# Optimization experiments

Measured on AMD Instinct MI355X. Metric: run time of the kernel, lower is better.

## Reference

```python
import jax, jax.numpy as jnp
import numpy as np

N = 100000   # nodes
D = 128      # embedding dim
E = 1600000  # edges (avg in-degree 16)
EPS = 1e-15
MAX_TANH_ARG = 1.0 - 1e-7  # keep arctanh finite


def _logmap0(x):
    # Poincare-ball logmap at the origin: artanh(||x||) * x / ||x||
    norm = jnp.linalg.norm(x, axis=-1, keepdims=True)
    safe = jnp.maximum(norm, EPS)
    return jnp.arctanh(jnp.clip(norm, 0.0, MAX_TANH_ARG)) * x / safe


def _expmap0(v):
    # Poincare-ball expmap at the origin: tanh(||v||) * v / ||v||
    norm = jnp.linalg.norm(v, axis=-1, keepdims=True)
    safe = jnp.maximum(norm, EPS)
    return jnp.tanh(norm) * v / safe


def setup_inputs() -> dict:
    key = jax.random.key(0)
    k1, k2, k3, k4, k5 = jax.random.split(key, 5)
    # small norms keep points strictly inside the unit ball
    x = jax.random.normal(k1, (N, D), dtype=jnp.float32) * 0.01
    src = jax.random.randint(k2, (E,), 0, N)
    dst = jax.random.randint(k3, (E,), 0, N)
    W = jax.random.normal(k4, (D, D), dtype=jnp.float32) * (1.0 / np.sqrt(D))
    b = jax.random.normal(k5, (D,), dtype=jnp.float32) * 0.01
    return {"x": x, "W": W, "b": b, "src": src, "dst": dst}


def reference(x, W, b, src, dst):
    # logmap to tangent space at origin
    tangent_x = _logmap0(x)
    # linear layer (nn.Linear: x @ W^T + b)
    h = tangent_x @ W.T + b  # [N, D]
    # copy_u + mean aggregation over in-neighbors (DGL update_all)
    msg_sum = jax.ops.segment_sum(h[src], dst, num_segments=N)      # [N, D]
    deg = jax.ops.segment_sum(jnp.ones((E,), h.dtype), dst, num_segments=N)
    neigh = msg_sum / jnp.maximum(deg, 1.0)[:, None]  # zero-degree nodes -> 0 (DGL mean)
    # expmap back onto the Poincare ball
    return _expmap0(neigh)
```

## Files before the change

### kernel.cpp

```cpp
#include <hip/hip_runtime.h>
#include <hip/hip_fp16.h>
#include <math.h>

constexpr int D = 128;
constexpr int BSH = 9;
constexpr int BNODES = 1 << BSH;
constexpr int NBLK = 256;

typedef __attribute__((ext_vector_type(8))) short bf16x8;
typedef __attribute__((ext_vector_type(4))) float f32x4;

__device__ inline short f2bf(float f) {
    unsigned u = __builtin_bit_cast(unsigned, f);
    u = (u + 0x7FFFu + ((u >> 16) & 1u)) >> 16;
    return (short)u;
}

__global__ __launch_bounds__(256) void hist_tangent_kernel(
    const int* __restrict__ dst, int* __restrict__ blkhist,
    int nEdges, int NB,
    const float* __restrict__ x, __half* __restrict__ th, int nNodes)
{
    __shared__ int hist[256];
    int t = threadIdx.x;

    if (blockIdx.x < NBLK) {
        hist[t] = 0;
        __syncthreads();
        int per = (nEdges + NBLK - 1) / NBLK;
        int i0 = blockIdx.x * per;
        int i1 = min(nEdges, i0 + per);
        for (int i = i0 + t; i < i1; i += 256)
            atomicAdd(&hist[dst[i] >> BSH], 1);
        __syncthreads();
        if (t < NB) blkhist[t * NBLK + blockIdx.x] = hist[t];
        return;
    }

    int nb = blockIdx.x - NBLK;
    int n    = (nb * 256 + t) >> 6;
    int lane = t & 63;
    if (n >= nNodes) return;
    float2 xv = *reinterpret_cast<const float2*>(x + (size_t)n * D + lane * 2);
    float ss = xv.x * xv.x + xv.y * xv.y;
    ss += __shfl_xor(ss, 1);
    ss += __shfl_xor(ss, 2);
    ss += __shfl_xor(ss, 4);
    ss += __shfl_xor(ss, 8);
    ss += __shfl_xor(ss, 16);
    ss += __shfl_xor(ss, 32);
    float norm = sqrtf(ss);
    float ncl  = fminf(norm, 1.0f - 1e-7f);
    float at   = 0.5f * logf((1.0f + ncl) / (1.0f - ncl));
    float sc   = at / fmaxf(norm, 1e-15f);
    __half2 h = __float22half2_rn(make_float2(xv.x * sc, xv.y * sc));
    *(reinterpret_cast<__half2*>(th + (size_t)n * D) + lane) = h;
}

__global__ __launch_bounds__(256) void part_scan1_kernel(
    int* __restrict__ blkhist, int* __restrict__ btot)
{
    __shared__ int s[256];
    int b = blockIdx.x;
    int t = threadIdx.x;
    int v = blkhist[b * NBLK + t];
    s[t] = v;
    __syncthreads();
    for (int off = 1; off < 256; off <<= 1) {
        int xv = (t >= off) ? s[t - off] : 0;
        __syncthreads();
        if (t >= off) s[t] += xv;
        __syncthreads();
    }
    blkhist[b * NBLK + t] = s[t] - v;
    if (t == 255) btot[b] = s[255];
}

__global__ __launch_bounds__(256) void part_scatter_kernel(
    const int* __restrict__ src, const int* __restrict__ dst,
    const int* __restrict__ blkhist, const int* __restrict__ btot,
    unsigned* __restrict__ part, int nEdges, int NB)
{
    __shared__ int sb[256];
    __shared__ int cur[256];
    int t = threadIdx.x;
    int v = (t < NB) ? btot[t] : 0;
    sb[t] = v;
    __syncthreads();
    for (int off = 1; off < 256; off <<= 1) {
        int xv = (t >= off) ? sb[t - off] : 0;
        __syncthreads();
        if (t >= off) sb[t] += xv;
        __syncthreads();
    }
    int bbase_t = sb[t] - v;
    cur[t] = (t < NB) ? (blkhist[t * NBLK + blockIdx.x] + bbase_t) : 0;
    __syncthreads();

    int per = (nEdges + gridDim.x - 1) / gridDim.x;
    int i0 = blockIdx.x * per;
    int i1 = min(nEdges, i0 + per);
    for (int i = i0 + t; i < i1; i += 256) {
        int d = dst[i];
        int b = d >> BSH;
        int p = atomicAdd(&cur[b], 1);
        part[p] = (unsigned)src[i] | ((unsigned)(d & (BNODES - 1)) << 17);
    }
}

__global__ __launch_bounds__(256) void bucket_csr_kernel(
    const unsigned* __restrict__ part, const int* __restrict__ btot,
    int* __restrict__ rowptr, float* __restrict__ degf,
    int* __restrict__ csr_src, int nNodes, int NB, int nEdges)
{
    __shared__ int cnt[BNODES];
    __shared__ int excl[BNODES];
    __shared__ int cur[BNODES];
    __shared__ int s[256];
    __shared__ int sBB[2];

    int b = blockIdx.x;
    int t = threadIdx.x;

    int v = (t < NB) ? btot[t] : 0;
    s[t] = v;
    __syncthreads();
    for (int off = 1; off < 256; off <<= 1) {
        int xv = (t >= off) ? s[t - off] : 0;
        __syncthreads();
        if (t >= off) s[t] += xv;
        __syncthreads();
    }
    if (t == b) { sBB[0] = s[t] - v; sBB[1] = s[t]; }
    __syncthreads();
    int bb = sBB[0], be = sBB[1];

    cnt[t] = 0; cnt[t + 256] = 0;
    cur[t] = 0; cur[t + 256] = 0;
    __syncthreads();

    for (int i = bb + t; i < be; i += 256)
        atomicAdd(&cnt[part[i] >> 17], 1);
    __syncthreads();

    int a0 = cnt[2 * t], a1 = cnt[2 * t + 1];
    s[t] = a0 + a1;
    __syncthreads();
    for (int off = 1; off < 256; off <<= 1) {
        int xv = (t >= off) ? s[t - off] : 0;
        __syncthreads();
        if (t >= off) s[t] += xv;
        __syncthreads();
    }
    int pbase = (t > 0) ? s[t - 1] : 0;
    excl[2 * t]     = pbase;
    excl[2 * t + 1] = pbase + a0;
    __syncthreads();

    int node0 = b << BSH;
#pragma unroll
    for (int q = 0; q < 2; ++q) {
        int j = t + q * 256;
        int d = node0 + j;
        if (d < nNodes) {
            rowptr[d] = bb + excl[j];
            degf[d]   = (float)cnt[j];
        }
    }
    if (b == NB - 1 && t == 0) rowptr[nNodes] = nEdges;

    for (int i = bb + t; i < be; i += 256) {
        unsigned vv = part[i];
        int dloc = vv >> 17;
        int p = bb + excl[dloc] + atomicAdd(&cur[dloc], 1);
        csr_src[p] = (int)(vv & 0x1FFFFu);
    }
}

__global__ __launch_bounds__(256) void hist_win_kernel(
    const int* __restrict__ dst, int* __restrict__ count,
    int nEdges, int winSize)
{
    int pass    = blockIdx.x & 7;
    int slice   = blockIdx.x >> 3;
    int nSlices = gridDim.x >> 3;
    int lo = pass * winSize;
    int hi = lo + winSize;

    int stride = nSlices * blockDim.x;
    for (int i = slice * blockDim.x + threadIdx.x; i < nEdges; i += stride) {
        int d = dst[i];
        if (d >= lo && d < hi) atomicAdd(&count[d], 1);
    }
}

__global__ __launch_bounds__(256) void scan_block_kernel(
    const int* __restrict__ count, int* __restrict__ rowptr,
    int* __restrict__ blksums, int n)
{
    __shared__ int sums[256];
    int t = threadIdx.x;
    int base = blockIdx.x * 1024 + t * 4;
    int v[4];
    int s = 0;
#pragma unroll
    for (int j = 0; j < 4; ++j) { v[j] = (base + j < n) ? count[base + j] : 0; s += v[j]; }
    sums[t] = s;
    __syncthreads();
    for (int off = 1; off < 256; off <<= 1) {
        int xv = (t >= off) ? sums[t - off] : 0;
        __syncthreads();
        if (t >= off) sums[t] += xv;
        __syncthreads();
    }
    int run = (t > 0) ? sums[t - 1] : 0;
#pragma unroll
    for (int j = 0; j < 4; ++j) { if (base + j < n) rowptr[base + j] = run; run += v[j]; }
    if (t == 255) blksums[blockIdx.x] = sums[255];
}

__global__ __launch_bounds__(256) void scan_totals_kernel(
    int* __restrict__ blksums, int* __restrict__ rowptr,
    int numBlocks, int n, int E)
{
    __shared__ int s[256];
    int t = threadIdx.x;
    s[t] = (t < numBlocks) ? blksums[t] : 0;
    __syncthreads();
    for (int off = 1; off < 256; off <<= 1) {
        int xv = (t >= off) ? s[t - off] : 0;
        __syncthreads();
        if (t >= off) s[t] += xv;
        __syncthreads();
    }
    if (t < numBlocks) blksums[t] = (t > 0) ? s[t - 1] : 0;
    if (t == 0) rowptr[n] = E;
}

__global__ __launch_bounds__(256) void add_offsets_kernel(
    int* __restrict__ rowptr, const int* __restrict__ blksums, int n)
{
    int i = blockIdx.x * 256 + threadIdx.x;
    if (i < n) rowptr[i] += blksums[i >> 10];
}

__global__ __launch_bounds__(256) void fill_win_kernel(
    const int* __restrict__ src, const int* __restrict__ dst,
    const int* __restrict__ rowptr, int* __restrict__ count,
    int* __restrict__ csr_src, int nEdges, int winSize)
{
    int pass    = blockIdx.x & 7;
    int slice   = blockIdx.x >> 3;
    int nSlices = gridDim.x >> 3;
    int lo = pass * winSize;
    int hi = lo + winSize;

    int stride = nSlices * blockDim.x;
    for (int i = slice * blockDim.x + threadIdx.x; i < nEdges; i += stride) {
        int d = dst[i];
        if (d >= lo && d < hi) {
            int pos = rowptr[d] + atomicSub(&count[d], 1) - 1;
            csr_src[pos] = src[i];
        }
    }
}

__global__ __launch_bounds__(256) void deg_from_rowptr_kernel(
    const int* __restrict__ rowptr, float* __restrict__ degf, int n)
{
    int i = blockIdx.x * 256 + threadIdx.x;
    if (i < n) degf[i] = (float)(rowptr[i + 1] - rowptr[i]);
}

__global__ __launch_bounds__(256) void scale_kernel(
    const float* __restrict__ x, float* __restrict__ scale, int nNodes)
{
    int node = (blockIdx.x * 256 + threadIdx.x) >> 6;
    int lane = threadIdx.x & 63;
    if (node >= nNodes) return;
    float2 xv = *reinterpret_cast<const float2*>(x + (size_t)node * D + lane * 2);
    float ss = xv.x * xv.x + xv.y * xv.y;
    ss += __shfl_xor(ss, 1);
    ss += __shfl_xor(ss, 2);
    ss += __shfl_xor(ss, 4);
    ss += __shfl_xor(ss, 8);
    ss += __shfl_xor(ss, 16);
    ss += __shfl_xor(ss, 32);
    if (lane == 0) {
        float norm = sqrtf(ss);
        float ncl  = fminf(norm, 1.0f - 1e-7f);
        float at   = 0.5f * logf((1.0f + ncl) / (1.0f - ncl));
        scale[node] = at / fmaxf(norm, 1e-15f);
    }
}

__global__ __launch_bounds__(256) void gather2_h16b_kernel(
    const __half* __restrict__ th,
    const int* __restrict__ csr_src, const int* __restrict__ rowptr,
    short* __restrict__ msgb, int nNodes)
{
    int t    = threadIdx.x;
    int lane = t & 63;
    int wave = t >> 6;
    int grp  = lane >> 4;
    int np   = grp >> 1;
    int g2   = grp & 1;
    int sl   = lane & 15;

    int n  = blockIdx.x * 8 + wave * 2 + np;
    int nn = n < nNodes ? n : nNodes - 1;
    int beg = rowptr[nn];
    int cnt = rowptr[nn + 1] - beg;

    __half2 z = __float2half2_rn(0.0f);
    __half2 acc0[4] = {z, z, z, z};
    __half2 acc1[4] = {z, z, z, z};

    int k = g2;
    for (; k + 6 < cnt; k += 8) {
        int s0 = csr_src[beg + k];
        int s1 = csr_src[beg + k + 2];
        int s2 = csr_src[beg + k + 4];
        int s3 = csr_src[beg + k + 6];
        float4 r0 = *reinterpret_cast<const float4*>(th + (size_t)s0 * D + sl * 8);
        float4 r1 = *reinterpret_cast<const float4*>(th + (size_t)s1 * D + sl * 8);
        float4 r2 = *reinterpret_cast<const float4*>(th + (size_t)s2 * D + sl * 8);
        float4 r3 = *reinterpret_cast<const float4*>(th + (size_t)s3 * D + sl * 8);
        const __half2* h0 = reinterpret_cast<const __half2*>(&r0);
        const __half2* h1 = reinterpret_cast<const __half2*>(&r1);
        const __half2* h2 = reinterpret_cast<const __half2*>(&r2);
        const __half2* h3 = reinterpret_cast<const __half2*>(&r3);
#pragma unroll
        for (int j = 0; j < 4; ++j) {
            acc0[j] = __hadd2(acc0[j], h0[j]);
            acc1[j] = __hadd2(acc1[j], h1[j]);
            acc0[j] = __hadd2(acc0[j], h2[j]);
            acc1[j] = __hadd2(acc1[j], h3[j]);
        }
    }
    for (; k < cnt; k += 2) {
        int s0 = csr_src[beg + k];
        float4 r0 = *reinterpret_cast<const float4*>(th + (size_t)s0 * D + sl * 8);
        const __half2* h0 = reinterpret_cast<const __half2*>(&r0);
#pragma unroll
        for (int j = 0; j < 4; ++j) acc0[j] = __hadd2(acc0[j], h0[j]);
    }
#pragma unroll
    for (int j = 0; j < 4; ++j) {
        acc0[j] = __hadd2(acc0[j], acc1[j]);
        float fx = __shfl_xor(__builtin_bit_cast(float, acc0[j]), 16);
        acc0[j] = __hadd2(acc0[j], __builtin_bit_cast(__half2, fx));
    }
    if (g2 == 0 && n < nNodes) {
        short s8[8];
#pragma unroll
        for (int j = 0; j < 4; ++j) {
            float2 f = __half22float2(acc0[j]);
            s8[2 * j]     = f2bf(f.x);
            s8[2 * j + 1] = f2bf(f.y);
        }
        *reinterpret_cast<float4*>(msgb + (size_t)n * D + sl * 8) =
            *reinterpret_cast<float4*>(s8);
    }
}

__global__ __launch_bounds__(256) void gather_h16_kernel(
    const __half* __restrict__ th,
    const int* __restrict__ csr_src, const int* __restrict__ rowptr,
    float* __restrict__ msg, int nNodes)
{
    int n    = blockIdx.x * 4 + (threadIdx.x >> 6);
    int lane = threadIdx.x & 63;
    if (n >= nNodes) return;
    int grp = lane >> 4;
    int sl  = lane & 15;

    int beg = rowptr[n];
    int cnt = rowptr[n + 1] - beg;

    __half2 z = __float2half2_rn(0.0f);
    __half2 acc0[4] = {z, z, z, z};
    __half2 acc1[4] = {z, z, z, z};

    int k = grp;
    for (; k + 12 < cnt; k += 16) {
        int s0 = csr_src[beg + k];
        int s1 = csr_src[beg + k + 4];
        int s2 = csr_src[beg + k + 8];
        int s3 = csr_src[beg + k + 12];
        float4 r0 = *reinterpret_cast<const float4*>(th + (size_t)s0 * D + sl * 8);
        float4 r1 = *reinterpret_cast<const float4*>(th + (size_t)s1 * D + sl * 8);
        float4 r2 = *reinterpret_cast<const float4*>(th + (size_t)s2 * D + sl * 8);
        float4 r3 = *reinterpret_cast<const float4*>(th + (size_t)s3 * D + sl * 8);
        const __half2* h0 = reinterpret_cast<const __half2*>(&r0);
        const __half2* h1 = reinterpret_cast<const __half2*>(&r1);
        const __half2* h2 = reinterpret_cast<const __half2*>(&r2);
        const __half2* h3 = reinterpret_cast<const __half2*>(&r3);
#pragma unroll
        for (int j = 0; j < 4; ++j) {
            acc0[j] = __hadd2(acc0[j], h0[j]);
            acc1[j] = __hadd2(acc1[j], h1[j]);
            acc0[j] = __hadd2(acc0[j], h2[j]);
            acc1[j] = __hadd2(acc1[j], h3[j]);
        }
    }
    for (; k < cnt; k += 4) {
        int s0 = csr_src[beg + k];
        float4 r0 = *reinterpret_cast<const float4*>(th + (size_t)s0 * D + sl * 8);
        const __half2* h0 = reinterpret_cast<const __half2*>(&r0);
#pragma unroll
        for (int j = 0; j < 4; ++j) acc0[j] = __hadd2(acc0[j], h0[j]);
    }
#pragma unroll
    for (int j = 0; j < 4; ++j) {
        acc0[j] = __hadd2(acc0[j], acc1[j]);
        float f16 = __shfl_xor(__builtin_bit_cast(float, acc0[j]), 16);
        acc0[j] = __hadd2(acc0[j], __builtin_bit_cast(__half2, f16));
        float f32v = __shfl_xor(__builtin_bit_cast(float, acc0[j]), 32);
        acc0[j] = __hadd2(acc0[j], __builtin_bit_cast(__half2, f32v));
    }
    if (grp == 0) {
        float2 f0 = __half22float2(acc0[0]);
        float2 f1 = __half22float2(acc0[1]);
        float2 f2 = __half22float2(acc0[2]);
        float2 f3 = __half22float2(acc0[3]);
        float4 o0 = make_float4(f0.x, f0.y, f1.x, f1.y);
        float4 o1 = make_float4(f2.x, f2.y, f3.x, f3.y);
        *reinterpret_cast<float4*>(msg + (size_t)n * D + sl * 8)     = o0;
        *reinterpret_cast<float4*>(msg + (size_t)n * D + sl * 8 + 4) = o1;
    }
}

__global__ __launch_bounds__(256) void gather_kernel(
    const float* __restrict__ x, const float* __restrict__ scale,
    const int* __restrict__ csr_src, const int* __restrict__ rowptr,
    float* __restrict__ msg, float* __restrict__ degf, int nNodes)
{
    int n    = blockIdx.x * 4 + (threadIdx.x >> 6);
    int lane = threadIdx.x & 63;
    if (n >= nNodes) return;

    int beg = rowptr[n], end = rowptr[n + 1];
    float2 acc0 = make_float2(0.0f, 0.0f);
    float2 acc1 = make_float2(0.0f, 0.0f);
    int e = beg;
    for (; e + 3 < end; e += 4) {
        int s0 = csr_src[e],     s1 = csr_src[e + 1];
        int s2 = csr_src[e + 2], s3 = csr_src[e + 3];
        float sc0 = scale[s0], sc1 = scale[s1];
        float sc2 = scale[s2], sc3 = scale[s3];
        float2 a = *reinterpret_cast<const float2*>(x + (size_t)s0 * D + lane * 2);
        float2 b = *reinterpret_cast<const float2*>(x + (size_t)s1 * D + lane * 2);
        float2 c = *reinterpret_cast<const float2*>(x + (size_t)s2 * D + lane * 2);
        float2 d = *reinterpret_cast<const float2*>(x + (size_t)s3 * D + lane * 2);
        acc0.x += sc0 * a.x;  acc0.y += sc0 * a.y;
        acc1.x += sc1 * b.x;  acc1.y += sc1 * b.y;
        acc0.x += sc2 * c.x;  acc0.y += sc2 * c.y;
        acc1.x += sc3 * d.x;  acc1.y += sc3 * d.y;
    }
    for (; e < end; ++e) {
        int s0 = csr_src[e];
        float sc0 = scale[s0];
        float2 a = *reinterpret_cast<const float2*>(x + (size_t)s0 * D + lane * 2);
        acc0.x += sc0 * a.x;  acc0.y += sc0 * a.y;
    }
    acc0.x += acc1.x;  acc0.y += acc1.y;
    *reinterpret_cast<float2*>(msg + (size_t)n * D + lane * 2) = acc0;
    if (lane == 0) degf[n] = (float)(end - beg);
}

__global__ __launch_bounds__(256) void edge_scatter_kernel(
    const float* __restrict__ x,
    const int* __restrict__ src,
    const int* __restrict__ dst,
    float* __restrict__ msg,
    float* __restrict__ deg,
    int nEdges)
{
    long long t = (long long)blockIdx.x * blockDim.x + threadIdx.x;
    int edge = (int)(t >> 5);
    int lane = (int)(t & 31);
    if (edge >= nEdges) return;

    int s = src[edge];
    int d = dst[edge];

    const float4 xv = *reinterpret_cast<const float4*>(x + (size_t)s * D + lane * 4);
    float ss = xv.x * xv.x + xv.y * xv.y + xv.z * xv.z + xv.w * xv.w;
    ss += __shfl_xor(ss, 1);
    ss += __shfl_xor(ss, 2);
    ss += __shfl_xor(ss, 4);
    ss += __shfl_xor(ss, 8);
    ss += __shfl_xor(ss, 16);

    float norm = sqrtf(ss);
    float ncl  = fminf(norm, 1.0f - 1e-7f);
    float at   = 0.5f * logf((1.0f + ncl) / (1.0f - ncl));
    float scale = at / fmaxf(norm, 1e-15f);

    float* mrow = msg + (size_t)d * D + lane * 4;
    unsafeAtomicAdd(mrow + 0, xv.x * scale);
    unsafeAtomicAdd(mrow + 1, xv.y * scale);
    unsafeAtomicAdd(mrow + 2, xv.z * scale);
    unsafeAtomicAdd(mrow + 3, xv.w * scale);
    if (lane == 0) unsafeAtomicAdd(deg + d, 1.0f);
}

__global__ __launch_bounds__(256) void gemm_mfma_b_kernel(
    const short* __restrict__ msgb, const float* __restrict__ deg,
    const float* __restrict__ W, const float* __restrict__ bias,
    float* __restrict__ out, int nNodes)
{
    __shared__ short sW[128][136];

    const int t = threadIdx.x;

#pragma unroll
    for (int p = 0; p < 16; ++p) {
        int chunk = p * 256 + t;
        int row = chunk >> 5;
        int c4  = (chunk & 31) * 4;
        float4 v = *reinterpret_cast<const float4*>(W + row * 128 + c4);
        short4 s;
        s.x = f2bf(v.x); s.y = f2bf(v.y); s.z = f2bf(v.z); s.w = f2bf(v.w);
        *reinterpret_cast<short4*>(&sW[row][c4]) = s;
    }
    __syncthreads();

    const int wave = t >> 6;
    const int lane = t & 63;
    const int l15  = lane & 15;
    const int lhi  = lane >> 4;
    const int m0   = blockIdx.x * 64 + wave * 16;

    int arow = m0 + l15;
    if (arow >= nNodes) arow = nNodes - 1;
    const short* ap = msgb + (size_t)arow * D + lhi * 8;
    bf16x8 a[4];
#pragma unroll
    for (int kc = 0; kc < 4; ++kc)
        a[kc] = *reinterpret_cast<const bf16x8*>(ap + kc * 32);

    f32x4 acc[8];
#pragma unroll
    for (int ct = 0; ct < 8; ++ct) acc[ct] = (f32x4){0.f, 0.f, 0.f, 0.f};

#pragma unroll
    for (int ct = 0; ct < 8; ++ct) {
#pragma unroll
        for (int kc = 0; kc < 4; ++kc) {
            bf16x8 bfrag = *reinterpret_cast<const bf16x8*>(
                &sW[ct * 16 + l15][kc * 32 + lhi * 8]);
            acc[ct] = __builtin_amdgcn_mfma_f32_16x16x32_bf16(a[kc], bfrag, acc[ct], 0, 0, 0);
        }
    }

    float bv[8];
#pragma unroll
    for (int ct = 0; ct < 8; ++ct) bv[ct] = bias[ct * 16 + l15];

#pragma unroll
    for (int r = 0; r < 4; ++r) {
        int row = m0 + lhi * 4 + r;
        int rc  = row < nNodes ? row : nNodes - 1;
        float dg  = deg[rc];
        float inv = 1.0f / fmaxf(dg, 1.0f);
        float v[8];
        float ss = 0.0f;
#pragma unroll
        for (int ct = 0; ct < 8; ++ct) {
            v[ct] = acc[ct][r] * inv + bv[ct];
            ss += v[ct] * v[ct];
        }
        ss += __shfl_xor(ss, 1);
        ss += __shfl_xor(ss, 2);
        ss += __shfl_xor(ss, 4);
        ss += __shfl_xor(ss, 8);
        float norm = sqrtf(ss);
        float sc = (dg > 0.0f) ? (tanhf(norm) / fmaxf(norm, 1e-15f)) : 0.0f;
        if (row < nNodes) {
#pragma unroll
            for (int ct = 0; ct < 8; ++ct)
                out[(size_t)row * D + ct * 16 + l15] = v[ct] * sc;
        }
    }
}

__global__ __launch_bounds__(256) void gemm_mfma_kernel(
    const float* msg, const float* __restrict__ deg,
    const float* __restrict__ W, const float* __restrict__ bias,
    float* out, int nNodes)
{
    __shared__ short sW[128][136];

    const int t = threadIdx.x;

#pragma unroll
    for (int p = 0; p < 16; ++p) {
        int chunk = p * 256 + t;
        int row = chunk >> 5;
        int c4  = (chunk & 31) * 4;
        float4 v = *reinterpret_cast<const float4*>(W + row * 128 + c4);
        short4 s;
        s.x = f2bf(v.x); s.y = f2bf(v.y); s.z = f2bf(v.z); s.w = f2bf(v.w);
        *reinterpret_cast<short4*>(&sW[row][c4]) = s;
    }
    __syncthreads();

    const int wave = t >> 6;
    const int lane = t & 63;
    const int l15  = lane & 15;
    const int lhi  = lane >> 4;
    const int m0   = blockIdx.x * 64 + wave * 16;

    int arow = m0 + l15;
    if (arow >= nNodes) arow = nNodes - 1;
    const float* ap = msg + (size_t)arow * D + lhi * 8;
    bf16x8 a[4];
#pragma unroll
    for (int kc = 0; kc < 4; ++kc) {
        float4 v0 = *reinterpret_cast<const float4*>(ap + kc * 32);
        float4 v1 = *reinterpret_cast<const float4*>(ap + kc * 32 + 4);
        bf16x8 f;
        f[0] = f2bf(v0.x); f[1] = f2bf(v0.y); f[2] = f2bf(v0.z); f[3] = f2bf(v0.w);
        f[4] = f2bf(v1.x); f[5] = f2bf(v1.y); f[6] = f2bf(v1.z); f[7] = f2bf(v1.w);
        a[kc] = f;
    }

    f32x4 acc[8];
#pragma unroll
    for (int ct = 0; ct < 8; ++ct) acc[ct] = (f32x4){0.f, 0.f, 0.f, 0.f};

#pragma unroll
    for (int ct = 0; ct < 8; ++ct) {
#pragma unroll
        for (int kc = 0; kc < 4; ++kc) {
            bf16x8 bfrag = *reinterpret_cast<const bf16x8*>(
                &sW[ct * 16 + l15][kc * 32 + lhi * 8]);
            acc[ct] = __builtin_amdgcn_mfma_f32_16x16x32_bf16(a[kc], bfrag, acc[ct], 0, 0, 0);
        }
    }

    float bv[8];
#pragma unroll
    for (int ct = 0; ct < 8; ++ct) bv[ct] = bias[ct * 16 + l15];

#pragma unroll
    for (int r = 0; r < 4; ++r) {
        int row = m0 + lhi * 4 + r;
        int rc  = row < nNodes ? row : nNodes - 1;
        float dg  = deg[rc];
        float inv = 1.0f / fmaxf(dg, 1.0f);
        float v[8];
        float ss = 0.0f;
#pragma unroll
        for (int ct = 0; ct < 8; ++ct) {
            v[ct] = acc[ct][r] * inv + bv[ct];
            ss += v[ct] * v[ct];
        }
        ss += __shfl_xor(ss, 1);
        ss += __shfl_xor(ss, 2);
        ss += __shfl_xor(ss, 4);
        ss += __shfl_xor(ss, 8);
        float norm = sqrtf(ss);
        float sc = (dg > 0.0f) ? (tanhf(norm) / fmaxf(norm, 1e-15f)) : 0.0f;
        if (row < nNodes) {
#pragma unroll
            for (int ct = 0; ct < 8; ++ct)
                out[(size_t)row * D + ct * 16 + l15] = v[ct] * sc;
        }
    }
}

static inline size_t align256(size_t o) { return (o + 255) & ~(size_t)255; }

extern "C" void kernel_launch(void* const* d_in, const int* in_sizes, int n_in,
                              void* d_out, int out_size, void* d_ws, size_t ws_size,
                              hipStream_t stream) {
    const float* x   = (const float*)d_in[0];
    const float* W   = (const float*)d_in[1];
    const float* b   = (const float*)d_in[2];
    const int*   src = (const int*)d_in[3];
    const int*   dst = (const int*)d_in[4];
    float* out = (float*)d_out;

    int nNodes = in_sizes[0] / D;
    int nEdges = in_sizes[3];
    int NB = (nNodes + BNODES - 1) >> BSH;

    char* ws = (char*)d_ws;
    size_t off = 0;
    float* degf    = (float*)(ws + off); off = align256(off + sizeof(float) * nNodes);
    int*   count   = (int*)  (ws + off); off = align256(off + sizeof(int) * nNodes);
    int*   rowptr  = (int*)  (ws + off); off = align256(off + sizeof(int) * (nNodes + 1));
    float* scl     = (float*)(ws + off); off = align256(off + sizeof(float) * nNodes);
    int*   blksums = (int*)  (ws + off); off = align256(off + sizeof(int) * 256);
    int*   btot    = (int*)  (ws + off); off = align256(off + sizeof(int) * 256);
    int*   blkhist = (int*)  (ws + off); off = align256(off + sizeof(int) * NBLK * 256);
    int*   csr_src = (int*)  (ws + off); off = align256(off + sizeof(int) * nEdges);
    size_t need_mid = off;

    size_t part_sz = sizeof(unsigned) * (size_t)nEdges;
    size_t msgb_sz = sizeof(short) * (size_t)nNodes * D;
    size_t th_sz   = sizeof(__half) * (size_t)nNodes * D;

    unsigned* part = (unsigned*)(ws + off);
    short*    msgb = (short*)   (ws + off);
    size_t off_lo = align256(off + part_sz);
    size_t off_hi = align256(off + (part_sz > msgb_sz ? part_sz : msgb_sz));
    __half* th_lo = (__half*)(ws + off_lo);
    __half* th_hi = (__half*)(ws + off_hi);
    size_t need_lo = align256(off_lo + th_sz);
    size_t need_hi = align256(off_hi + th_sz);

    float* msg = out;

    int numScanBlocks = (nNodes + 1023) / 1024;
    bool part_ok = (ws_size >= need_lo) && (nNodes <= 131072) && (NB <= 256);
    bool bf16msg = (ws_size >= need_hi) && (nNodes <= 131072) && (NB <= 256);
    bool mid_ok  = (ws_size >= need_mid) && (numScanBlocks <= 256);

    if (part_ok || bf16msg) {
        __half* th = bf16msg ? th_hi : th_lo;
        int TB = (nNodes + 3) / 4;
        hist_tangent_kernel<<<NBLK + TB, 256, 0, stream>>>(
            dst, blkhist, nEdges, NB, x, th, nNodes);
        part_scan1_kernel<<<NB, 256, 0, stream>>>(blkhist, btot);
        part_scatter_kernel<<<NBLK, 256, 0, stream>>>(src, dst, blkhist, btot, part, nEdges, NB);
        bucket_csr_kernel<<<NB, 256, 0, stream>>>(part, btot, rowptr, degf,
                                                  csr_src, nNodes, NB, nEdges);
        if (bf16msg) {
            gather2_h16b_kernel<<<(nNodes + 7) / 8, 256, 0, stream>>>(th, csr_src, rowptr, msgb, nNodes);
            gemm_mfma_b_kernel<<<(nNodes + 63) / 64, 256, 0, stream>>>(msgb, degf, W, b, out, nNodes);
        } else {
            gather_h16_kernel<<<(nNodes + 3) / 4, 256, 0, stream>>>(th, csr_src, rowptr, msg, nNodes);
            gemm_mfma_kernel<<<(nNodes + 63) / 64, 256, 0, stream>>>(msg, degf, W, b, out, nNodes);
        }
        return;
    }

    if (mid_ok) {
        hipMemsetAsync(count, 0, sizeof(int) * nNodes, stream);
        int winSize = (nNodes + 7) / 8;
        hist_win_kernel<<<4096, 256, 0, stream>>>(dst, count, nEdges, winSize);
        scan_block_kernel<<<numScanBlocks, 256, 0, stream>>>(count, rowptr, blksums, nNodes);
        scan_totals_kernel<<<1, 256, 0, stream>>>(blksums, rowptr, numScanBlocks, nNodes, nEdges);
        add_offsets_kernel<<<(nNodes + 255) / 256, 256, 0, stream>>>(rowptr, blksums, nNodes);
        fill_win_kernel<<<4096, 256, 0, stream>>>(src, dst, rowptr, count, csr_src, nEdges, winSize);
        deg_from_rowptr_kernel<<<(nNodes + 255) / 256, 256, 0, stream>>>(rowptr, degf, nNodes);

        scale_kernel<<<(nNodes + 3) / 4, 256, 0, stream>>>(x, scl, nNodes);
        gather_kernel<<<(nNodes + 3) / 4, 256, 0, stream>>>(x, scl, csr_src, rowptr, msg, degf, nNodes);
        gemm_mfma_kernel<<<(nNodes + 63) / 64, 256, 0, stream>>>(msg, degf, W, b, out, nNodes);
        return;
    }

    {
        float* deg = (float*)d_ws;
        hipMemsetAsync(msg, 0, (size_t)nNodes * D * sizeof(float), stream);
        hipMemsetAsync(deg, 0, (size_t)nNodes * sizeof(float), stream);
        long long threads = (long long)nEdges * 32;
        int blocks = (int)((threads + 255) / 256);
        edge_scatter_kernel<<<blocks, 256, 0, stream>>>(x, src, dst, msg, (float*)d_ws, nEdges);
        gemm_mfma_kernel<<<(nNodes + 63) / 64, 256, 0, stream>>>(msg, (float*)d_ws, W, b, out, nNodes);
    }
}
```

Measured before the change: 140.7 us.

## Store tangent features as scaled fp8 to halve gather traffic

```diff
diff --git a/kernel.cpp b/kernel.cpp
--- a/kernel.cpp
+++ b/kernel.cpp
@@ -9,11 +9,54 @@
 
 typedef __attribute__((ext_vector_type(8))) short bf16x8;
 typedef __attribute__((ext_vector_type(4))) float f32x4;
+typedef __attribute__((ext_vector_type(2))) float f32x2;
 
 __device__ inline short f2bf(float f) {
     unsigned u = __builtin_bit_cast(unsigned, f);
     u = (u + 0x7FFFu + ((u >> 16) & 1u)) >> 16;
     return (short)u;
+}
+
+__global__ __launch_bounds__(256) void hist_tangent8_kernel(
+    const int* __restrict__ dst, int* __restrict__ blkhist,
+    int nEdges, int NB,
+    const float* __restrict__ x, unsigned char* __restrict__ th8, int nNodes)
+{
+    __shared__ int hist[256];
+    int t = threadIdx.x;
+
+    if (blockIdx.x < NBLK) {
+        hist[t] = 0;
+        __syncthreads();
+        int per = (nEdges + NBLK - 1) / NBLK;
+        int i0 = blockIdx.x * per;
+        int i1 = min(nEdges, i0 + per);
+        for (int i = i0 + t; i < i1; i += 256)
+            atomicAdd(&hist[dst[i] >> BSH], 1);
+        __syncthreads();
+        if (t < NB) blkhist[t * NBLK + blockIdx.x] = hist[t];
+        return;
+    }
+
+    int nb = blockIdx.x - NBLK;
+    int hw = t >> 5;
+    int l  = t & 31;
+    int n  = nb * 8 + hw;
+    if (n >= nNodes) return;
+    float4 xv = *reinterpret_cast<const float4*>(x + (size_t)n * D + l * 4);
+    float ss = xv.x * xv.x + xv.y * xv.y + xv.z * xv.z + xv.w * xv.w;
+    ss += __shfl_xor(ss, 1);
+    ss += __shfl_xor(ss, 2);
+    ss += __shfl_xor(ss, 4);
+    ss += __shfl_xor(ss, 8);
+    ss += __shfl_xor(ss, 16);
+    float norm = sqrtf(ss);
+    float ncl  = fminf(norm, 1.0f - 1e-7f);
+    float at   = 0.5f * logf((1.0f + ncl) / (1.0f - ncl));
+    float sc64 = 64.0f * at / fmaxf(norm, 1e-15f);
+    int u = __builtin_amdgcn_cvt_pk_fp8_f32(xv.x * sc64, xv.y * sc64, 0, false);
+    u     = __builtin_amdgcn_cvt_pk_fp8_f32(xv.z * sc64, xv.w * sc64, u, true);
+    reinterpret_cast<unsigned*>(th8 + (size_t)n * D)[l] = (unsigned)u;
 }
 
 __global__ __launch_bounds__(256) void hist_tangent_kernel(
@@ -294,73 +337,84 @@
     }
 }
 
-__global__ __launch_bounds__(256) void gather2_h16b_kernel(
-    const __half* __restrict__ th,
+__global__ __launch_bounds__(256) void gather8_kernel(
+    const unsigned char* __restrict__ th8,
     const int* __restrict__ csr_src, const int* __restrict__ rowptr,
     short* __restrict__ msgb, int nNodes)
 {
     int t    = threadIdx.x;
     int lane = t & 63;
     int wave = t >> 6;
-    int grp  = lane >> 4;
-    int np   = grp >> 1;
-    int g2   = grp & 1;
-    int sl   = lane & 15;
+    int np   = lane >> 5;
+    int rem  = lane & 31;
+    int g    = rem >> 3;
+    int sl   = rem & 7;
 
     int n  = blockIdx.x * 8 + wave * 2 + np;
     int nn = n < nNodes ? n : nNodes - 1;
     int beg = rowptr[nn];
     int cnt = rowptr[nn + 1] - beg;
 
-    __half2 z = __float2half2_rn(0.0f);
-    __half2 acc0[4] = {z, z, z, z};
-    __half2 acc1[4] = {z, z, z, z};
-
-    int k = g2;
-    for (; k + 6 < cnt; k += 8) {
+    float acc[16];
+#pragma unroll
+    for (int j = 0; j < 16; ++j) acc[j] = 0.0f;
+
+    int k = g;
+    for (; k + 12 < cnt; k += 16) {
         int s0 = csr_src[beg + k];
-        int s1 = csr_src[beg + k + 2];
-        int s2 = csr_src[beg + k + 4];
-        int s3 = csr_src[beg + k + 6];
-        float4 r0 = *reinterpret_cast<const float4*>(th + (size_t)s0 * D + sl * 8);
-        float4 r1 = *reinterpret_cast<const float4*>(th + (size_t)s1 * D + sl * 8);
-        float4 r2 = *reinterpret_cast<const float4*>(th + (size_t)s2 * D + sl * 8);
-        float4 r3 = *reinterpret_cast<const float4*>(th + (size_t)s3 * D + sl * 8);
-        const __half2* h0 = reinterpret_cast<const __half2*>(&r0);
-        const __half2* h1 = reinterpret_cast<const __half2*>(&r1);
-        const __half2* h2 = reinterpret_cast<const __half2*>(&r2);
-        const __half2* h3 = reinterpret_cast<const __half2*>(&r3);
-#pragma unroll
-        for (int j = 0; j < 4; ++j) {
-            acc0[j] = __hadd2(acc0[j], h0[j]);
-            acc1[j] = __hadd2(acc1[j], h1[j]);
-            acc0[j] = __hadd2(acc0[j], h2[j]);
-            acc1[j] = __hadd2(acc1[j], h3[j]);
-        }
-    }
-    for (; k < cnt; k += 2) {
+        int s1 = csr_src[beg + k + 4];
+        int s2 = csr_src[beg + k + 8];
+        int s3 = csr_src[beg + k + 12];
+        float4 r0 = *reinterpret_cast<const float4*>(th8 + (size_t)s0 * D + sl * 16);
+        float4 r1 = *reinterpret_cast<const float4*>(th8 + (size_t)s1 * D + sl * 16);
+        float4 r2 = *reinterpret_cast<const float4*>(th8 + (size_t)s2 * D + sl * 16);
+        float4 r3 = *reinterpret_cast<const float4*>(th8 + (size_t)s3 * D + sl * 16);
+        const unsigned* u0 = reinterpret_cast<const unsigned*>(&r0);
+        const unsigned* u1 = reinterpret_cast<const unsigned*>(&r1);
+        const unsigned* u2 = reinterpret_cast<const unsigned*>(&r2);
+        const unsigned* u3 = reinterpret_cast<const unsigned*>(&r3);
+#pragma unroll
+        for (int q = 0; q < 4; ++q) {
+            f32x2 a0 = __builtin_amdgcn_cvt_pk_f32_fp8(u0[q], false);
+            f32x2 b0 = __builtin_amdgcn_cvt_pk_f32_fp8(u0[q], true);
+            f32x2 a1 = __builtin_amdgcn_cvt_pk_f32_fp8(u1[q], false);
+            f32x2 b1 = __builtin_amdgcn_cvt_pk_f32_fp8(u1[q], true);
+            f32x2 a2 = __builtin_amdgcn_cvt_pk_f32_fp8(u2[q], false);
+            f32x2 b2 = __builtin_amdgcn_cvt_pk_f32_fp8(u2[q], true);
+            f32x2 a3 = __builtin_amdgcn_cvt_pk_f32_fp8(u3[q], false);
+            f32x2 b3 = __builtin_amdgcn_cvt_pk_f32_fp8(u3[q], true);
+            acc[4 * q + 0] += (a0[0] + a1[0]) + (a2[0] + a3[0]);
+            acc[4 * q + 1] += (a0[1] + a1[1]) + (a2[1] + a3[1]);
+            acc[4 * q + 2] += (b0[0] + b1[0]) + (b2[0] + b3[0]);
+            acc[4 * q + 3] += (b0[1] + b1[1]) + (b2[1] + b3[1]);
+        }
+    }
+    for (; k < cnt; k += 4) {
         int s0 = csr_src[beg + k];
-        float4 r0 = *reinterpret_cast<const float4*>(th + (size_t)s0 * D + sl * 8);
-        const __half2* h0 = reinterpret_cast<const __half2*>(&r0);
-#pragma unroll
-        for (int j = 0; j < 4; ++j) acc0[j] = __hadd2(acc0[j], h0[j]);
-    }
-#pragma unroll
-    for (int j = 0; j < 4; ++j) {
-        acc0[j] = __hadd2(acc0[j], acc1[j]);
-        float fx = __shfl_xor(__builtin_bit_cast(float, acc0[j]), 16);
-        acc0[j] = __hadd2(acc0[j], __builtin_bit_cast(__half2, fx));
-    }
-    if (g2 == 0 && n < nNodes) {
-        short s8[8];
-#pragma unroll
-        for (int j = 0; j < 4; ++j) {
-            float2 f = __half22float2(acc0[j]);
-            s8[2 * j]     = f2bf(f.x);
-            s8[2 * j + 1] = f2bf(f.y);
-        }
-        *reinterpret_cast<float4*>(msgb + (size_t)n * D + sl * 8) =
-            *reinterpret_cast<float4*>(s8);
+        float4 r0 = *reinterpret_cast<const float4*>(th8 + (size_t)s0 * D + sl * 16);
+        const unsigned* u0 = reinterpret_cast<const unsigned*>(&r0);
+#pragma unroll
+        for (int q = 0; q < 4; ++q) {
+            f32x2 a0 = __builtin_amdgcn_cvt_pk_f32_fp8(u0[q], false);
+            f32x2 b0 = __builtin_amdgcn_cvt_pk_f32_fp8(u0[q], true);
+            acc[4 * q + 0] += a0[0];
+            acc[4 * q + 1] += a0[1];
+            acc[4 * q + 2] += b0[0];
+            acc[4 * q + 3] += b0[1];
+        }
+    }
+#pragma unroll
+    for (int j = 0; j < 16; ++j) {
+        acc[j] += __shfl_xor(acc[j], 8);
+        acc[j] += __shfl_xor(acc[j], 16);
+    }
+    if (g == 0 && n < nNodes) {
+        short s16[16];
+#pragma unroll
+        for (int j = 0; j < 16; ++j) s16[j] = f2bf(acc[j]);
+        float4* o = reinterpret_cast<float4*>(msgb + (size_t)n * D + sl * 16);
+        o[0] = reinterpret_cast<float4*>(s16)[0];
+        o[1] = reinterpret_cast<float4*>(s16)[1];
     }
 }
 
@@ -564,7 +618,7 @@
         int row = m0 + lhi * 4 + r;
         int rc  = row < nNodes ? row : nNodes - 1;
         float dg  = deg[rc];
-        float inv = 1.0f / fmaxf(dg, 1.0f);
+        float inv = 1.0f / (64.0f * fmaxf(dg, 1.0f));
         float v[8];
         float ss = 0.0f;
 #pragma unroll
@@ -702,38 +756,44 @@
 
     size_t part_sz = sizeof(unsigned) * (size_t)nEdges;
     size_t msgb_sz = sizeof(short) * (size_t)nNodes * D;
-    size_t th_sz   = sizeof(__half) * (size_t)nNodes * D;
+    size_t th8_sz  = sizeof(unsigned char) * (size_t)nNodes * D;
+    size_t th16_sz = sizeof(__half) * (size_t)nNodes * D;
 
     unsigned* part = (unsigned*)(ws + off);
     short*    msgb = (short*)   (ws + off);
     size_t off_lo = align256(off + part_sz);
     size_t off_hi = align256(off + (part_sz > msgb_sz ? part_sz : msgb_sz));
-    __half* th_lo = (__half*)(ws + off_lo);
-    __half* th_hi = (__half*)(ws + off_hi);
-    size_t need_lo = align256(off_lo + th_sz);
-    size_t need_hi = align256(off_hi + th_sz);
+    __half*        th_lo = (__half*)(ws + off_lo);
+    unsigned char* th8   = (unsigned char*)(ws + off_hi);
+    size_t need_lo = align256(off_lo + th16_sz);
+    size_t need_hi = align256(off_hi + th8_sz);
 
     float* msg = out;
 
     int numScanBlocks = (nNodes + 1023) / 1024;
     bool part_ok = (ws_size >= need_lo) && (nNodes <= 131072) && (NB <= 256);
-    bool bf16msg = (ws_size >= need_hi) && (nNodes <= 131072) && (NB <= 256);
+    bool fp8msg  = (ws_size >= need_hi) && (nNodes <= 131072) && (NB <= 256);
     bool mid_ok  = (ws_size >= need_mid) && (numScanBlocks <= 256);
 
-    if (part_ok || bf16msg) {
-        __half* th = bf16msg ? th_hi : th_lo;
-        int TB = (nNodes + 3) / 4;
-        hist_tangent_kernel<<<NBLK + TB, 256, 0, stream>>>(
-            dst, blkhist, nEdges, NB, x, th, nNodes);
+    if (part_ok || fp8msg) {
+        if (fp8msg) {
+            int TB = (nNodes + 7) / 8;
+            hist_tangent8_kernel<<<NBLK + TB, 256, 0, stream>>>(
+                dst, blkhist, nEdges, NB, x, th8, nNodes);
+        } else {
+            int TB = (nNodes + 3) / 4;
+            hist_tangent_kernel<<<NBLK + TB, 256, 0, stream>>>(
+                dst, blkhist, nEdges, NB, x, th_lo, nNodes);
+        }
         part_scan1_kernel<<<NB, 256, 0, stream>>>(blkhist, btot);
         part_scatter_kernel<<<NBLK, 256, 0, stream>>>(src, dst, blkhist, btot, part, nEdges, NB);
         bucket_csr_kernel<<<NB, 256, 0, stream>>>(part, btot, rowptr, degf,
                                                   csr_src, nNodes, NB, nEdges);
-        if (bf16msg) {
-            gather2_h16b_kernel<<<(nNodes + 7) / 8, 256, 0, stream>>>(th, csr_src, rowptr, msgb, nNodes);
+        if (fp8msg) {
+            gather8_kernel<<<(nNodes + 7) / 8, 256, 0, stream>>>(th8, csr_src, rowptr, msgb, nNodes);
             gemm_mfma_b_kernel<<<(nNodes + 63) / 64, 256, 0, stream>>>(msgb, degf, W, b, out, nNodes);
         } else {
-            gather_h16_kernel<<<(nNodes + 3) / 4, 256, 0, stream>>>(th, csr_src, rowptr, msg, nNodes);
+            gather_h16_kernel<<<(nNodes + 3) / 4, 256, 0, stream>>>(th_lo, csr_src, rowptr, msg, nNodes);
             gemm_mfma_kernel<<<(nNodes + 63) / 64, 256, 0, stream>>>(msg, degf, W, b, out, nNodes);
         }
         return;
```

Result: faster. 125.0 us, median of 3 (-11.2%).
